# Kernel tuning notes

Measured on AMD Instinct MI355X. Metric: run time of the kernel, lower is better.

## Reference

```python
import jax, jax.numpy as jnp
import numpy as np
from itertools import permutations

NODE, BATCH, DIM, STEP = 32, 64, 32, 8
E = NODE * (NODE - 1)          # 992 directed edges (all ordered pairs)
K = 3                          # edge types
MSG_HID = 64; MSG_OUT = 64; N_HID = 64; PRED_LEN = 8


def setup_inputs() -> dict:
    key = jax.random.key(0)
    ks = jax.random.split(key, 12)
    es = jnp.asarray(np.array(list(permutations(range(NODE), 2))).T, dtype=jnp.int32)  # [2, E]
    x = jax.random.normal(ks[0], (BATCH, NODE, DIM, STEP), jnp.float32)
    z = jax.nn.softmax(jax.random.normal(ks[1], (BATCH, E, K), jnp.float32), axis=-1)
    p = lambda k, shape: jax.random.normal(k, shape, jnp.float32) * 0.1
    return dict(
        x=x, z=z, es=es,
        nodes_mask=jnp.zeros((NODE,), jnp.float32),
        edges_mask=jnp.zeros((E,), jnp.float32),
        mask=jnp.zeros((1,), jnp.float32),
        msg_W1=p(ks[2], (K, 2 * DIM, MSG_HID)), msg_b1=jnp.zeros((K, MSG_HID), jnp.float32),
        msg_W2=p(ks[3], (K, MSG_HID, MSG_OUT)), msg_b2=jnp.zeros((K, MSG_OUT), jnp.float32),
        out_W1=p(ks[4], (DIM + MSG_OUT, N_HID)), out_b1=jnp.zeros((N_HID,), jnp.float32),
        out_W2=p(ks[5], (N_HID, N_HID)), out_b2=jnp.zeros((N_HID,), jnp.float32),
        out_W3=p(ks[6], (N_HID, DIM)), out_b3=jnp.zeros((DIM,), jnp.float32),
        ge_Wi=p(ks[7], (3, N_HID, N_HID)), ge_bi=jnp.zeros((3, N_HID), jnp.float32),
        ge_Wh=p(ks[8], (3, N_HID, N_HID)), ge_bh=jnp.zeros((3, N_HID), jnp.float32),
        gn_Wi=p(ks[9], (3, N_HID + DIM, N_HID + DIM)), gn_bi=jnp.zeros((3, N_HID + DIM), jnp.float32),
        gn_Wh=p(ks[10], (3, N_HID + DIM, N_HID + DIM)), gn_bh=jnp.zeros((3, N_HID + DIM), jnp.float32),
    )


def _gru(inp, hid, Wi, bi, Wh, bh):
    # GRUX: state defaults to hidden
    r = jax.nn.sigmoid(inp @ Wi[0] + bi[0] + hid @ Wh[0] + bh[0])
    i = jax.nn.sigmoid(inp @ Wi[1] + bi[1] + hid @ Wh[1] + bh[1])
    n = jnp.tanh(inp @ Wi[2] + bi[2] + r * (hid @ Wh[2] + bh[2]))
    return (1.0 - i) * n + i * hid


def _run(x, z, es, msg_W1, msg_b1, msg_W2, msg_b2,
         out_W1, out_b1, out_W2, out_b2, out_W3, out_b3,
         ge_Wi, ge_bi, ge_Wh, ge_bh, gn_Wi, gn_bi, gn_Wh, gn_bh):
    xp = jnp.transpose(x, (1, 0, 3, 2))   # [node, batch, step, dim]
    zp = jnp.transpose(z, (1, 0, 2))      # [E, batch, K]
    col, row = es[0], es[1]               # 'o2i': col,row = es; aggregate at col
    counts = jnp.clip(jax.ops.segment_sum(jnp.ones((E,), x.dtype), col, num_segments=NODE), 1.0)
    h_node = h_edge = None
    x_m = None
    xs = []
    for t in range(STEP + PRED_LEN):
        x_in = xp[:, :, t, :] if t < STEP else x_m   # [node, batch, dim]
        # edge gather: msg = cat([x[row], x[col]])
        msg = jnp.concatenate([x_in[row], x_in[col]], axis=-1)  # [E, b, 2*dim]
        # per-edge-type 2-layer MLP mixture, weighted by z, normalized by K
        h1 = jax.nn.relu(jnp.einsum('ebi,kih->kebh', msg, msg_W1) + msg_b1[:, None, None, :])
        h2 = jax.nn.relu(jnp.einsum('kebh,kho->kebo', h1, msg_W2) + msg_b2[:, None, None, :])
        msgs = jnp.einsum('kebo,ebk->ebo', h2, zp) / K          # [E, b, msg_out]
        if h_edge is not None:
            msgs = _gru(msgs, h_edge, ge_Wi, ge_bi, ge_Wh, ge_bh)
        # scatter-mean to nodes
        agg = jax.ops.segment_sum(msgs, col, num_segments=NODE) / counts[:, None, None]
        cat = jnp.concatenate([x_in, agg], axis=-1)             # [node, b, dim+msg_out]
        if h_node is not None:
            cat = _gru(cat, h_node, gn_Wi, gn_bi, gn_Wh, gn_bh)
        h = jax.nn.relu(cat @ out_W1 + out_b1)
        h = jax.nn.relu(h @ out_W2 + out_b2)
        delta = h @ out_W3 + out_b3
        x_m = x_in + delta
        h_node, h_edge = cat, msgs
        xs.append(x_m)
    x_hat = jnp.transpose(jnp.stack(xs, axis=2), (1, 0, 3, 2))  # [batch, node, dim, T]
    return x_hat


def reference(x, z, es, nodes_mask, edges_mask, mask,
              msg_W1, msg_b1, msg_W2, msg_b2,
              out_W1, out_b1, out_W2, out_b2, out_W3, out_b3,
              ge_Wi, ge_bi, ge_Wh, ge_bh, gn_Wi, gn_bi, gn_Wh, gn_bh):
    x_hat = _run(x, z, es, msg_W1, msg_b1, msg_W2, msg_b2,
                 out_W1, out_b1, out_W2, out_b2, out_W3, out_b3,
                 ge_Wi, ge_bi, ge_Wh, ge_bh, gn_Wi, gn_bi, gn_Wh, gn_bh)
    return (x_hat[:, :, :, -PRED_LEN:], x_hat, x_hat)
```

## Files before the change

kernel.cpp:

```cpp
#include <hip/hip_runtime.h>
#include <hip/hip_bf16.h>

#define NNODE 32
#define NB    64
#define NDIM  32
#define NSTEP 8
#define NE    992
#define NTT   16

typedef __bf16 bf16;
typedef __attribute__((ext_vector_type(8))) __bf16 bf16x8;
typedef __attribute__((ext_vector_type(4))) __bf16 bf16x4;
typedef __attribute__((ext_vector_type(4))) float  f32x4;

__device__ __forceinline__ f32x4 mfma_bf16(bf16x8 a, bf16x8 b, f32x4 c) {
  return __builtin_amdgcn_mfma_f32_16x16x32_bf16(a, b, c, 0, 0, 0);
}
__device__ __forceinline__ float sigm(float x) { return 1.0f / (1.0f + __expf(-x)); }
__device__ __forceinline__ float tanh_f(float x) {
  x = fminf(fmaxf(x, -15.0f), 15.0f);
  float e = __expf(2.0f * x);
  return (e - 1.0f) / (e + 1.0f);
}

__global__ void prep_weights(
    const float* __restrict__ msgW1, const float* __restrict__ msgW2,
    const float* __restrict__ geWi,  const float* __restrict__ geWh,
    const float* __restrict__ gnWi,  const float* __restrict__ gnWh,
    const float* __restrict__ oW1,   const float* __restrict__ oW2,
    const float* __restrict__ oW3,
    bf16* __restrict__ B1, bf16* __restrict__ B2,
    bf16* __restrict__ GI, bf16* __restrict__ GH,
    bf16* __restrict__ GN,
    bf16* __restrict__ OW1s, bf16* __restrict__ OW2s, bf16* __restrict__ OW3s) {
  int u = blockIdx.x * 256 + threadIdx.x;
  if (u < 12288) {
    int k = u >> 12, i = (u >> 6) & 63, h = u & 63;
    int kf = i >> 5, quad = (i >> 3) & 3, j = i & 7;
    int nn = k * 64 + h, nt = nn >> 4, lane = quad * 16 + (nn & 15);
    int slot = ((nt * 2 + kf) * 64 + lane) * 8 + j;
    B1[slot] = (bf16)msgW1[u];
    GI[slot] = (bf16)geWi[u];
    GH[slot] = (bf16)geWh[u];
    int ntl = h >> 4, lane2 = quad * 16 + (h & 15);
    int slot2 = k * 4096 + ((ntl * 2 + kf) * 64 + lane2) * 8 + j;
    B2[slot2] = (bf16)msgW2[u];
  } else if (u < 39936) {
    int v = u - 12288;
    int kk = v / 9216, rem = v % 9216, i = rem / 96, h = rem % 96;
    int kf = i >> 5, loc = i & 31, quad = loc >> 3, j = loc & 7;
    int nn = kk * 96 + h, nt = nn >> 4, lane = quad * 16 + (nn & 15);
    int slot = ((nt * 3 + kf) * 64 + lane) * 8 + j;
    GN[slot]         = (bf16)gnWi[v];
    GN[27648 + slot] = (bf16)gnWh[v];
  } else if (u < 46080) {
    int v = u - 39936; int i = v >> 6, h = v & 63;
    int kf = i >> 5, loc = i & 31, quad = loc >> 3, j = loc & 7;
    int nt = h >> 4, lane = quad * 16 + (h & 15);
    OW1s[((nt * 3 + kf) * 64 + lane) * 8 + j] = (bf16)oW1[v];
  } else if (u < 50176) {
    int v = u - 46080; int i = v >> 6, h = v & 63;
    int kf = i >> 5, quad = (i >> 3) & 3, j = i & 7;
    int nt = h >> 4, lane = quad * 16 + (h & 15);
    OW2s[((nt * 2 + kf) * 64 + lane) * 8 + j] = (bf16)oW2[v];
  } else if (u < 52224) {
    int v = u - 50176; int i = v >> 5, h = v & 31;
    int kf = i >> 5, quad = (i >> 3) & 3, j = i & 7;
    int nt = h >> 4, lane = quad * 16 + (h & 15);
    OW3s[((nt * 2 + kf) * 64 + lane) * 8 + j] = (bf16)oW3[v];
  }
}

__global__ void copy_x(const float* __restrict__ x, float* __restrict__ xf,
                       bf16* __restrict__ xb) {
  int u = blockIdx.x * 256 + threadIdx.x;
  int n = u >> 11, b = (u >> 5) & 63, d = u & 31;
  float v = x[((b * 32 + n) * 32 + d) * 8 + 0];
  xf[u] = v;
  xb[u] = (bf16)v;
}

__global__ __launch_bounds__(512, 4) void edge_step(
    const bf16* __restrict__ xb, const int* __restrict__ es,
    const float* __restrict__ z,
    const bf16* __restrict__ B1, const bf16* __restrict__ B2,
    const float* __restrict__ mb1, const float* __restrict__ mb2,
    const bf16* __restrict__ GI, const bf16* __restrict__ GH,
    const float* __restrict__ gbi, const float* __restrict__ gbh,
    bf16* __restrict__ hed, int t) {
  __shared__ __align__(16) char scrbuf[51200];
  __shared__ float zL[2][64][3];
  __shared__ __align__(16) bf16 Hh[2][64][72];
  bf16 (*A)[64][72]   = (bf16(*)[64][72])scrbuf;
  bf16 (*A2)[64][200] = (bf16(*)[64][200])scrbuf;

  int e0 = blockIdx.x * 2, tid = threadIdx.x;
  int c0_ = es[e0],     r0 = es[NE + e0];
  int c1_ = es[e0 + 1], r1 = es[NE + e0 + 1];
  int wv = tid >> 6, ln = tid & 63, quad = ln >> 4, l16 = ln & 15;
  int rg = wv & 3, cg = wv >> 2;
  int m = rg * 16 + l16;

  for (int u = tid; u < 384; u += 512) {
    int pe = u / 192, rem = u % 192, b = rem / 3, k = rem % 3;
    zL[pe][b][k] = z[(b * NE + e0 + pe) * 3 + k];
  }
  if (t > 0) {
    for (int u = tid; u < 1024; u += 512) {
      int pe = u >> 9, c = u & 511;
      int b = c >> 3, j = c & 7;
      *(bf16x8*)&Hh[pe][b][j * 8] =
          *(const bf16x8*)(hed + (e0 + pe) * 4096 + b * 64 + j * 8);
    }
  }

  bf16x8 af[2][2];
  af[0][0] = *(const bf16x8*)(xb + r0 * 2048 + m * 32 + quad * 8);
  af[0][1] = *(const bf16x8*)(xb + c0_ * 2048 + m * 32 + quad * 8);
  af[1][0] = *(const bf16x8*)(xb + r1 * 2048 + m * 32 + quad * 8);
  af[1][1] = *(const bf16x8*)(xb + c1_ * 2048 + m * 32 + quad * 8);

  f32x4 acc1[2][6];
#pragma unroll
  for (int pe = 0; pe < 2; pe++)
#pragma unroll
    for (int q = 0; q < 6; q++) { f32x4 zz = {0.f,0.f,0.f,0.f}; acc1[pe][q] = zz; }
#pragma unroll
  for (int j = 0; j < 6; j++) {
    int nt = cg * 6 + j;
    bf16x8 w0 = *(const bf16x8*)&B1[(nt * 2 + 0) * 512 + ln * 8];
    bf16x8 w1 = *(const bf16x8*)&B1[(nt * 2 + 1) * 512 + ln * 8];
#pragma unroll
    for (int pe = 0; pe < 2; pe++) {
      acc1[pe][j] = mfma_bf16(af[pe][0], w0, acc1[pe][j]);
      acc1[pe][j] = mfma_bf16(af[pe][1], w1, acc1[pe][j]);
    }
  }
#pragma unroll
  for (int j = 0; j < 6; j++) {
    int nt = cg * 6 + j;
    int n = nt * 16 + l16;
    float bias = mb1[n];
#pragma unroll
    for (int pe = 0; pe < 2; pe++)
#pragma unroll
      for (int r = 0; r < 4; r++) {
        float v = acc1[pe][j][r] + bias;
        A2[pe][rg * 16 + quad * 4 + r][n] = (bf16)(v > 0.f ? v : 0.f);
      }
  }
  __syncthreads();
  f32x4 acc2[2][3][2];
#pragma unroll
  for (int pe = 0; pe < 2; pe++)
#pragma unroll
    for (int kt = 0; kt < 3; kt++)
#pragma unroll
      for (int oi = 0; oi < 2; oi++) { f32x4 zz = {0.f,0.f,0.f,0.f}; acc2[pe][kt][oi] = zz; }
#pragma unroll
  for (int kt = 0; kt < 3; kt++) {
    bf16x8 a2f[2][2];
#pragma unroll
    for (int pe = 0; pe < 2; pe++)
#pragma unroll
      for (int kf = 0; kf < 2; kf++)
        a2f[pe][kf] = *(const bf16x8*)&A2[pe][m][kt * 64 + kf * 32 + quad * 8];
#pragma unroll
    for (int oi = 0; oi < 2; oi++) {
      int ot = cg * 2 + oi;
      bf16x8 w0 = *(const bf16x8*)&B2[kt * 4096 + (ot * 2 + 0) * 512 + ln * 8];
      bf16x8 w1 = *(const bf16x8*)&B2[kt * 4096 + (ot * 2 + 1) * 512 + ln * 8];
#pragma unroll
      for (int pe = 0; pe < 2; pe++) {
        acc2[pe][kt][oi] = mfma_bf16(a2f[pe][0], w0, acc2[pe][kt][oi]);
        acc2[pe][kt][oi] = mfma_bf16(a2f[pe][1], w1, acc2[pe][kt][oi]);
      }
    }
  }
  __syncthreads();
  float mb2v[3][2];
#pragma unroll
  for (int kt = 0; kt < 3; kt++)
#pragma unroll
    for (int oi = 0; oi < 2; oi++)
      mb2v[kt][oi] = mb2[kt * 64 + (cg * 2 + oi) * 16 + l16];
#pragma unroll
  for (int pe = 0; pe < 2; pe++)
#pragma unroll
    for (int r = 0; r < 4; r++) {
      int b = rg * 16 + quad * 4 + r;
      float z0 = zL[pe][b][0], z1 = zL[pe][b][1], z2 = zL[pe][b][2];
#pragma unroll
      for (int oi = 0; oi < 2; oi++) {
        int o = (cg * 2 + oi) * 16 + l16;
        float h0 = acc2[pe][0][oi][r] + mb2v[0][oi]; h0 = h0 > 0.f ? h0 : 0.f;
        float h1 = acc2[pe][1][oi][r] + mb2v[1][oi]; h1 = h1 > 0.f ? h1 : 0.f;
        float h2 = acc2[pe][2][oi][r] + mb2v[2][oi]; h2 = h2 > 0.f ? h2 : 0.f;
        float val = (h0 * z0 + h1 * z1 + h2 * z2) * (1.0f / 3.0f);
        if (t == 0)
          hed[(e0 + pe) * 4096 + b * 64 + o] = (bf16)val;
        else
          A[pe][b][o] = (bf16)val;
      }
    }
  if (t > 0) {
    __syncthreads();
    bf16x8 ai[2][2], ah[2][2];
#pragma unroll
    for (int pe = 0; pe < 2; pe++)
#pragma unroll
      for (int kf = 0; kf < 2; kf++) {
        ai[pe][kf] = *(const bf16x8*)&A[pe][m][kf * 32 + quad * 8];
        ah[pe][kf] = *(const bf16x8*)&Hh[pe][m][kf * 32 + quad * 8];
      }
#pragma unroll
    for (int oi = 0; oi < 2; oi++) {
      int ot = cg * 2 + oi;
      f32x4 gr[2], gi2[2], gni2[2], gnh2[2];
#pragma unroll
      for (int pe = 0; pe < 2; pe++) {
        f32x4 zz = {0.f,0.f,0.f,0.f};
        gr[pe] = zz; gi2[pe] = zz; gni2[pe] = zz; gnh2[pe] = zz;
      }
#pragma unroll
      for (int g = 0; g < 2; g++) {
        int nt = g * 4 + ot;
        bf16x8 wi0 = *(const bf16x8*)&GI[(nt * 2 + 0) * 512 + ln * 8];
        bf16x8 wi1 = *(const bf16x8*)&GI[(nt * 2 + 1) * 512 + ln * 8];
        bf16x8 wh0 = *(const bf16x8*)&GH[(nt * 2 + 0) * 512 + ln * 8];
        bf16x8 wh1 = *(const bf16x8*)&GH[(nt * 2 + 1) * 512 + ln * 8];
#pragma unroll
        for (int pe = 0; pe < 2; pe++) {
          f32x4 a = g ? gi2[pe] : gr[pe];
          a = mfma_bf16(ai[pe][0], wi0, a);
          a = mfma_bf16(ai[pe][1], wi1, a);
          a = mfma_bf16(ah[pe][0], wh0, a);
          a = mfma_bf16(ah[pe][1], wh1, a);
          if (g) gi2[pe] = a; else gr[pe] = a;
        }
      }
      {
        int nt = 8 + ot;
        bf16x8 wi0 = *(const bf16x8*)&GI[(nt * 2 + 0) * 512 + ln * 8];
        bf16x8 wi1 = *(const bf16x8*)&GI[(nt * 2 + 1) * 512 + ln * 8];
        bf16x8 wh0 = *(const bf16x8*)&GH[(nt * 2 + 0) * 512 + ln * 8];
        bf16x8 wh1 = *(const bf16x8*)&GH[(nt * 2 + 1) * 512 + ln * 8];
#pragma unroll
        for (int pe = 0; pe < 2; pe++) {
          gni2[pe] = mfma_bf16(ai[pe][0], wi0, gni2[pe]);
          gni2[pe] = mfma_bf16(ai[pe][1], wi1, gni2[pe]);
          gnh2[pe] = mfma_bf16(ah[pe][0], wh0, gnh2[pe]);
          gnh2[pe] = mfma_bf16(ah[pe][1], wh1, gnh2[pe]);
        }
      }
      int o = ot * 16 + l16;
      float bir = gbi[o],       bhr = gbh[o];
      float bii = gbi[64 + o],  bhi = gbh[64 + o];
      float bin = gbi[128 + o], bhn = gbh[128 + o];
#pragma unroll
      for (int pe = 0; pe < 2; pe++)
#pragma unroll
        for (int r = 0; r < 4; r++) {
          int b = rg * 16 + quad * 4 + r;
          float xr = gr[pe][r]   + bir + bhr;
          float xi = gi2[pe][r]  + bii + bhi;
          float xn = gni2[pe][r] + bin;
          float hn = gnh2[pe][r] + bhn;
          float rgt = sigm(xr);
          float ig  = sigm(xi);
          float ng  = tanh_f(xn + rgt * hn);
          float hv  = (float)Hh[pe][b][o];
          hed[(e0 + pe) * 4096 + b * 64 + o] =
              (bf16)((1.0f - ig) * ng + ig * hv);
        }
    }
  }
}

__global__ __launch_bounds__(256) void node_kernel(
    const float* __restrict__ x, const bf16* __restrict__ hed,
    float* __restrict__ xf, bf16* __restrict__ xb, float* __restrict__ hnode,
    const bf16* __restrict__ GN,
    const float* __restrict__ gnbi, const float* __restrict__ gnbh,
    const bf16* __restrict__ OW1, const float* __restrict__ ob1,
    const bf16* __restrict__ OW2, const float* __restrict__ ob2,
    const bf16* __restrict__ OW3, const float* __restrict__ ob3,
    float* __restrict__ out, int t) {
  __shared__ float aggf[16][64];
  __shared__ float xinf[16][32];
  __shared__ float hvf[16][96];
  __shared__ __align__(16) bf16 c0b[16][112];
  __shared__ __align__(16) bf16 hvb[16][112];
  __shared__ float gsum[2][16][290];
  __shared__ __align__(16) bf16 cnb[16][112];
  __shared__ __align__(16) bf16 s1b[16][112];
  __shared__ __align__(16) bf16 s2b[16][112];
  int nq = blockIdx.x, n = nq >> 2, q = nq & 3;
  int tid = threadIdx.x;
  {
    int r = tid >> 4, o4 = tid & 15;
    const bf16x4* bp = (const bf16x4*)hed + (size_t)n * 31 * 1024 + (q * 16 + r) * 16 + o4;
    float sx = 0.f, sy = 0.f, sz = 0.f, sw = 0.f;
#pragma unroll
    for (int e2 = 0; e2 < 31; e2++) {
      bf16x4 v = bp[e2 * 1024];
      sx += (float)v[0]; sy += (float)v[1]; sz += (float)v[2]; sw += (float)v[3];
    }
    const float inv = 1.0f / 31.0f;
    sx *= inv; sy *= inv; sz *= inv; sw *= inv;
    int o = o4 * 4;
    aggf[r][o] = sx; aggf[r][o + 1] = sy; aggf[r][o + 2] = sz; aggf[r][o + 3] = sw;
    c0b[r][32 + o] = (bf16)sx; c0b[r][33 + o] = (bf16)sy;
    c0b[r][34 + o] = (bf16)sz; c0b[r][35 + o] = (bf16)sw;
  }
  if (tid < 128) {
    int r = tid >> 3, d0 = (tid & 7) * 4;
    int b = q * 16 + r;
#pragma unroll
    for (int k = 0; k < 4; k++) {
      float v = xf[n * 2048 + b * 32 + d0 + k];
      xinf[r][d0 + k] = v;
      c0b[r][d0 + k] = (bf16)v;
    }
  }
  if (t > 0) {
    int r = tid >> 4, cb = (tid & 15) * 6;
    int row = n * 64 + q * 16 + r;
#pragma unroll
    for (int k = 0; k < 6; k++) {
      float v = hnode[row * 96 + cb + k];
      hvf[r][cb + k] = v;
      hvb[r][cb + k] = (bf16)v;
    }
  }
  __syncthreads();
  int wv = tid >> 6, ln = tid & 63, quad = ln >> 4, l16 = ln & 15;
  if (t > 0) {
    int mat = wv >> 1, sel = wv & 1;
    const bf16(*Ab)[112] = mat ? hvb : c0b;
    bf16x8 af[3];
#pragma unroll
    for (int kf = 0; kf < 3; kf++)
      af[kf] = *(const bf16x8*)&Ab[l16][kf * 32 + quad * 8];
    const bf16* W = GN + mat * 27648;
    f32x4 accn[9];
#pragma unroll
    for (int q2 = 0; q2 < 9; q2++) { f32x4 zz = {0.f,0.f,0.f,0.f}; accn[q2] = zz; }
#pragma unroll
    for (int nt2 = 0; nt2 < 9; nt2++) {
      int nt = sel * 9 + nt2;
#pragma unroll
      for (int kf = 0; kf < 3; kf++) {
        bf16x8 bfrag = *(const bf16x8*)&W[((nt * 3 + kf) * 64 + ln) * 8];
        accn[nt2] = mfma_bf16(af[kf], bfrag, accn[nt2]);
      }
    }
#pragma unroll
    for (int nt2 = 0; nt2 < 9; nt2++) {
      int col = (sel * 9 + nt2) * 16 + l16;
#pragma unroll
      for (int rr = 0; rr < 4; rr++)
        gsum[mat][quad * 4 + rr][col] = accn[nt2][rr];
    }
  }
  __syncthreads();
  {
    int r = tid >> 4, cb = (tid & 15) * 6;
    int row = n * 64 + q * 16 + r;
#pragma unroll
    for (int k = 0; k < 6; k++) {
      int c = cb + k;
      float v;
      if (t > 0) {
        float xr = gsum[0][r][c] + gnbi[c] + gsum[1][r][c] + gnbh[c];
        float xi = gsum[0][r][96 + c] + gnbi[96 + c] + gsum[1][r][96 + c] + gnbh[96 + c];
        float xn = gsum[0][r][192 + c] + gnbi[192 + c];
        float hn = gsum[1][r][192 + c] + gnbh[192 + c];
        float rg = sigm(xr);
        float ig = sigm(xi);
        float ng = tanh_f(xn + rg * hn);
        v = (1.0f - ig) * ng + ig * hvf[r][c];
      } else {
        v = (c < 32) ? xinf[r][c] : aggf[r][c - 32];
      }
      cnb[r][c] = (bf16)v;
      hnode[row * 96 + c] = v;
    }
  }
  __syncthreads();
  {
    bf16x8 af3[3];
#pragma unroll
    for (int kf = 0; kf < 3; kf++)
      af3[kf] = *(const bf16x8*)&cnb[l16][kf * 32 + quad * 8];
    f32x4 accn = {0.f, 0.f, 0.f, 0.f};
#pragma unroll
    for (int kf = 0; kf < 3; kf++) {
      bf16x8 bfrag = *(const bf16x8*)&OW1[((wv * 3 + kf) * 64 + ln) * 8];
      accn = mfma_bf16(af3[kf], bfrag, accn);
    }
    int col = wv * 16 + l16;
    float bias = ob1[col];
#pragma unroll
    for (int rr = 0; rr < 4; rr++) {
      float vv = accn[rr] + bias;
      s1b[quad * 4 + rr][col] = (bf16)(vv > 0.f ? vv : 0.f);
    }
  }
  __syncthreads();
  {
    bf16x8 af2[2];
#pragma unroll
    for (int kf = 0; kf < 2; kf++)
      af2[kf] = *(const bf16x8*)&s1b[l16][kf * 32 + quad * 8];
    f32x4 accn = {0.f, 0.f, 0.f, 0.f};
#pragma unroll
    for (int kf = 0; kf < 2; kf++) {
      bf16x8 bfrag = *(const bf16x8*)&OW2[((wv * 2 + kf) * 64 + ln) * 8];
      accn = mfma_bf16(af2[kf], bfrag, accn);
    }
    int col = wv * 16 + l16;
    float bias = ob2[col];
#pragma unroll
    for (int rr = 0; rr < 4; rr++) {
      float vv = accn[rr] + bias;
      s2b[quad * 4 + rr][col] = (bf16)(vv > 0.f ? vv : 0.f);
    }
  }
  __syncthreads();
  if (wv < 2) {
    bf16x8 af2[2];
#pragma unroll
    for (int kf = 0; kf < 2; kf++)
      af2[kf] = *(const bf16x8*)&s2b[l16][kf * 32 + quad * 8];
    f32x4 accn = {0.f, 0.f, 0.f, 0.f};
#pragma unroll
    for (int kf = 0; kf < 2; kf++) {
      bf16x8 bfrag = *(const bf16x8*)&OW3[((wv * 2 + kf) * 64 + ln) * 8];
      accn = mfma_bf16(af2[kf], bfrag, accn);
    }
    int d = wv * 16 + l16;
    float bias = ob3[d];
#pragma unroll
    for (int rr = 0; rr < 4; rr++) {
      int r = quad * 4 + rr;
      int b = q * 16 + r;
      float xm = xinf[r][d] + accn[rr] + bias;
      int base = (b * 32 + n) * 32 + d;
      out[524288 + base * 16 + t] = xm;
      out[1572864 + base * 16 + t] = xm;
      if (t >= NSTEP) out[base * 8 + (t - NSTEP)] = xm;
      float vnext = (t + 1 < NSTEP) ? x[base * 8 + (t + 1)] : xm;
      xf[n * 2048 + b * 32 + d] = vnext;
      xb[n * 2048 + b * 32 + d] = (bf16)vnext;
    }
  }
}

extern "C" void kernel_launch(void* const* d_in, const int* in_sizes, int n_in,
                              void* d_out, int out_size, void* d_ws, size_t ws_size,
                              hipStream_t stream) {
  const float* x     = (const float*)d_in[0];
  const float* z     = (const float*)d_in[1];
  const int*   es    = (const int*)d_in[2];
  const float* msgW1 = (const float*)d_in[6];
  const float* msgb1 = (const float*)d_in[7];
  const float* msgW2 = (const float*)d_in[8];
  const float* msgb2 = (const float*)d_in[9];
  const float* oW1   = (const float*)d_in[10];
  const float* ob1   = (const float*)d_in[11];
  const float* oW2   = (const float*)d_in[12];
  const float* ob2   = (const float*)d_in[13];
  const float* oW3   = (const float*)d_in[14];
  const float* ob3   = (const float*)d_in[15];
  const float* geWi  = (const float*)d_in[16];
  const float* gebi  = (const float*)d_in[17];
  const float* geWh  = (const float*)d_in[18];
  const float* gebh  = (const float*)d_in[19];
  const float* gnWi  = (const float*)d_in[20];
  const float* gnbi  = (const float*)d_in[21];
  const float* gnWh  = (const float*)d_in[22];
  const float* gnbh  = (const float*)d_in[23];
  float* out = (float*)d_out;

  char* p = (char*)d_ws;
  bf16*  hed   = (bf16*)p;   p += (size_t)NE * 4096 * 2;
  float* xf    = (float*)p;  p += 65536 * 4;
  bf16*  xb    = (bf16*)p;   p += 65536 * 2;
  float* hnode = (float*)p;  p += 196608 * 4;
  bf16*  B1sw  = (bf16*)p;   p += 12288 * 2;
  bf16*  B2sw  = (bf16*)p;   p += 12288 * 2;
  bf16*  GIsw  = (bf16*)p;   p += 12288 * 2;
  bf16*  GHsw  = (bf16*)p;   p += 12288 * 2;
  bf16*  GNsw  = (bf16*)p;   p += 55296 * 2;
  bf16*  OW1s  = (bf16*)p;   p += 6144 * 2;
  bf16*  OW2s  = (bf16*)p;   p += 4096 * 2;
  bf16*  OW3s  = (bf16*)p;   p += 2048 * 2;

  prep_weights<<<204, 256, 0, stream>>>(msgW1, msgW2, geWi, geWh, gnWi, gnWh,
                                        oW1, oW2, oW3,
                                        B1sw, B2sw, GIsw, GHsw, GNsw,
                                        OW1s, OW2s, OW3s);
  copy_x<<<256, 256, 0, stream>>>(x, xf, xb);

  for (int t = 0; t < NTT; t++) {
    edge_step<<<NE / 2, 512, 0, stream>>>(xb, es, z, B1sw, B2sw, msgb1, msgb2,
                                          GIsw, GHsw, gebi, gebh, hed, t);
    node_kernel<<<128, 256, 0, stream>>>(x, hed, xf, xb, hnode, GNsw, gnbi, gnbh,
                                         OW1s, ob1, OW2s, ob2, OW3s, ob3,
                                         out, t);
  }
}
```

Baseline: 599.7 us.

## Fuse edge-to-node scatter-sum into edge kernel via float atomics

The edge kernel now atomically adds each bf16-rounded edge message into a float per-node aggregation buffer, indexed by the edge's target node. The node kernel then reads one float4 from that buffer, instead of summing 31 edge messages from the hed array, and zeroes it for the next step. The buffer is zeroed once in copy_x. This removes the 31-way strided gather from the node kernel. In exchange the edge kernel issues about 4M contended float atomics per step, and float atomic order makes the summation order nondeterministic.

```diff
diff --git a/kernel.cpp b/kernel.cpp
--- a/kernel.cpp
+++ b/kernel.cpp
@@ -72,8 +72,10 @@
 }
 
 __global__ void copy_x(const float* __restrict__ x, float* __restrict__ xf,
-                       bf16* __restrict__ xb) {
+                       bf16* __restrict__ xb, float* __restrict__ agg) {
   int u = blockIdx.x * 256 + threadIdx.x;
+  agg[u] = 0.f;
+  agg[u + 65536] = 0.f;
   int n = u >> 11, b = (u >> 5) & 63, d = u & 31;
   float v = x[((b * 32 + n) * 32 + d) * 8 + 0];
   xf[u] = v;
@@ -87,7 +89,7 @@
     const float* __restrict__ mb1, const float* __restrict__ mb2,
     const bf16* __restrict__ GI, const bf16* __restrict__ GH,
     const float* __restrict__ gbi, const float* __restrict__ gbh,
-    bf16* __restrict__ hed, int t) {
+    bf16* __restrict__ hed, float* __restrict__ agg, int t) {
   __shared__ __align__(16) char scrbuf[51200];
   __shared__ float zL[2][64][3];
   __shared__ __align__(16) bf16 Hh[2][64][72];
@@ -197,10 +199,13 @@
         float h1 = acc2[pe][1][oi][r] + mb2v[1][oi]; h1 = h1 > 0.f ? h1 : 0.f;
         float h2 = acc2[pe][2][oi][r] + mb2v[2][oi]; h2 = h2 > 0.f ? h2 : 0.f;
         float val = (h0 * z0 + h1 * z1 + h2 * z2) * (1.0f / 3.0f);
-        if (t == 0)
-          hed[(e0 + pe) * 4096 + b * 64 + o] = (bf16)val;
-        else
+        if (t == 0) {
+          bf16 bv = (bf16)val;
+          hed[(e0 + pe) * 4096 + b * 64 + o] = bv;
+          atomicAdd(&agg[((pe ? c1_ : c0_) * 64 + b) * 64 + o], (float)bv);
+        } else {
           A[pe][b][o] = (bf16)val;
+        }
       }
     }
   if (t > 0) {
@@ -270,15 +275,16 @@
           float ig  = sigm(xi);
           float ng  = tanh_f(xn + rgt * hn);
           float hv  = (float)Hh[pe][b][o];
-          hed[(e0 + pe) * 4096 + b * 64 + o] =
-              (bf16)((1.0f - ig) * ng + ig * hv);
+          bf16 bv = (bf16)((1.0f - ig) * ng + ig * hv);
+          hed[(e0 + pe) * 4096 + b * 64 + o] = bv;
+          atomicAdd(&agg[((pe ? c1_ : c0_) * 64 + b) * 64 + o], (float)bv);
         }
     }
   }
 }
 
 __global__ __launch_bounds__(256) void node_kernel(
-    const float* __restrict__ x, const bf16* __restrict__ hed,
+    const float* __restrict__ x, float* __restrict__ agg,
     float* __restrict__ xf, bf16* __restrict__ xb, float* __restrict__ hnode,
     const bf16* __restrict__ GN,
     const float* __restrict__ gnbi, const float* __restrict__ gnbh,
@@ -299,15 +305,12 @@
   int tid = threadIdx.x;
   {
     int r = tid >> 4, o4 = tid & 15;
-    const bf16x4* bp = (const bf16x4*)hed + (size_t)n * 31 * 1024 + (q * 16 + r) * 16 + o4;
-    float sx = 0.f, sy = 0.f, sz = 0.f, sw = 0.f;
-#pragma unroll
-    for (int e2 = 0; e2 < 31; e2++) {
-      bf16x4 v = bp[e2 * 1024];
-      sx += (float)v[0]; sy += (float)v[1]; sz += (float)v[2]; sw += (float)v[3];
-    }
+    float* ap = agg + ((size_t)(n * 64) + q * 16 + r) * 64 + o4 * 4;
+    f32x4 s = *(const f32x4*)ap;
+    f32x4 zz = {0.f, 0.f, 0.f, 0.f};
+    *(f32x4*)ap = zz;
     const float inv = 1.0f / 31.0f;
-    sx *= inv; sy *= inv; sz *= inv; sw *= inv;
+    float sx = s[0] * inv, sy = s[1] * inv, sz = s[2] * inv, sw = s[3] * inv;
     int o = o4 * 4;
     aggf[r][o] = sx; aggf[r][o + 1] = sy; aggf[r][o + 2] = sz; aggf[r][o + 3] = sw;
     c0b[r][32 + o] = (bf16)sx; c0b[r][33 + o] = (bf16)sy;
@@ -488,6 +491,7 @@
   float* xf    = (float*)p;  p += 65536 * 4;
   bf16*  xb    = (bf16*)p;   p += 65536 * 2;
   float* hnode = (float*)p;  p += 196608 * 4;
+  float* agg   = (float*)p;  p += 131072 * 4;
   bf16*  B1sw  = (bf16*)p;   p += 12288 * 2;
   bf16*  B2sw  = (bf16*)p;   p += 12288 * 2;
   bf16*  GIsw  = (bf16*)p;   p += 12288 * 2;
@@ -501,12 +505,12 @@
                                         oW1, oW2, oW3,
                                         B1sw, B2sw, GIsw, GHsw, GNsw,
                                         OW1s, OW2s, OW3s);
-  copy_x<<<256, 256, 0, stream>>>(x, xf, xb);
+  copy_x<<<256, 256, 0, stream>>>(x, xf, xb, agg);
 
   for (int t = 0; t < NTT; t++) {
     edge_step<<<NE / 2, 512, 0, stream>>>(xb, es, z, B1sw, B2sw, msgb1, msgb2,
-                                          GIsw, GHsw, gebi, gebh, hed, t);
-    node_kernel<<<128, 256, 0, stream>>>(x, hed, xf, xb, hnode, GNsw, gnbi, gnbh,
+                                          GIsw, GHsw, gebi, gebh, hed, agg, t);
+    node_kernel<<<128, 256, 0, stream>>>(x, agg, xf, xb, hnode, GNsw, gnbi, gnbh,
                                          OW1s, ob1, OW2s, ob2, OW3s, ob3,
                                          out, t);
   }
```

Result: slower. 618.8 us (+3.2%).

## Fuse node step t-1 with edge step t during teacher-forced phase

Applied to the files above, without the earlier changes.

Because teacher-forced edge inputs come directly from x, the edge step for t no longer depends on the node step for t-1. The change double-buffers the edge hidden state, precomputes bf16 x for all input steps, and launches one fused kernel whose first blocks run node work while the rest run edge work. This aims to remove a launch and serialization gap per teacher-forced step and overlap the small node grid with edge work. It enlarges the static shared memory of edge blocks, which may lower occupancy, and adds a second hidden-state buffer.

```diff
diff --git a/kernel.cpp b/kernel.cpp
--- a/kernel.cpp
+++ b/kernel.cpp
@@ -72,29 +72,31 @@
 }
 
 __global__ void copy_x(const float* __restrict__ x, float* __restrict__ xf,
-                       bf16* __restrict__ xb) {
+                       bf16* __restrict__ xball) {
   int u = blockIdx.x * 256 + threadIdx.x;
   int n = u >> 11, b = (u >> 5) & 63, d = u & 31;
-  float v = x[((b * 32 + n) * 32 + d) * 8 + 0];
-  xf[u] = v;
-  xb[u] = (bf16)v;
-}
-
-__global__ __launch_bounds__(512, 4) void edge_step(
-    const bf16* __restrict__ xb, const int* __restrict__ es,
+  int base = ((b * 32 + n) * 32 + d) * 8;
+  xf[u] = x[base];
+#pragma unroll
+  for (int t = 0; t < 8; t++)
+    xball[t * 65536 + u] = (bf16)x[base + t];
+}
+
+__device__ __forceinline__ void edge_body(
+    char* smem, int e0, int tid,
+    const bf16* __restrict__ xsrc, const int* __restrict__ es,
     const float* __restrict__ z,
     const bf16* __restrict__ B1, const bf16* __restrict__ B2,
     const float* __restrict__ mb1, const float* __restrict__ mb2,
     const bf16* __restrict__ GI, const bf16* __restrict__ GH,
     const float* __restrict__ gbi, const float* __restrict__ gbh,
-    bf16* __restrict__ hed, int t) {
-  __shared__ __align__(16) char scrbuf[51200];
-  __shared__ float zL[2][64][3];
-  __shared__ __align__(16) bf16 Hh[2][64][72];
+    const bf16* __restrict__ hedR, bf16* __restrict__ hedW, int t) {
+  char* scrbuf = smem;
+  float (*zL)[64][3] = (float(*)[64][3])(smem + 51200);
+  bf16 (*Hh)[64][72] = (bf16(*)[64][72])(smem + 52736);
   bf16 (*A)[64][72]   = (bf16(*)[64][72])scrbuf;
   bf16 (*A2)[64][200] = (bf16(*)[64][200])scrbuf;
 
-  int e0 = blockIdx.x * 2, tid = threadIdx.x;
   int c0_ = es[e0],     r0 = es[NE + e0];
   int c1_ = es[e0 + 1], r1 = es[NE + e0 + 1];
   int wv = tid >> 6, ln = tid & 63, quad = ln >> 4, l16 = ln & 15;
@@ -110,15 +112,15 @@
       int pe = u >> 9, c = u & 511;
       int b = c >> 3, j = c & 7;
       *(bf16x8*)&Hh[pe][b][j * 8] =
-          *(const bf16x8*)(hed + (e0 + pe) * 4096 + b * 64 + j * 8);
+          *(const bf16x8*)(hedR + (e0 + pe) * 4096 + b * 64 + j * 8);
     }
   }
 
   bf16x8 af[2][2];
-  af[0][0] = *(const bf16x8*)(xb + r0 * 2048 + m * 32 + quad * 8);
-  af[0][1] = *(const bf16x8*)(xb + c0_ * 2048 + m * 32 + quad * 8);
-  af[1][0] = *(const bf16x8*)(xb + r1 * 2048 + m * 32 + quad * 8);
-  af[1][1] = *(const bf16x8*)(xb + c1_ * 2048 + m * 32 + quad * 8);
+  af[0][0] = *(const bf16x8*)(xsrc + r0 * 2048 + m * 32 + quad * 8);
+  af[0][1] = *(const bf16x8*)(xsrc + c0_ * 2048 + m * 32 + quad * 8);
+  af[1][0] = *(const bf16x8*)(xsrc + r1 * 2048 + m * 32 + quad * 8);
+  af[1][1] = *(const bf16x8*)(xsrc + c1_ * 2048 + m * 32 + quad * 8);
 
   f32x4 acc1[2][6];
 #pragma unroll
@@ -198,7 +200,7 @@
         float h2 = acc2[pe][2][oi][r] + mb2v[2][oi]; h2 = h2 > 0.f ? h2 : 0.f;
         float val = (h0 * z0 + h1 * z1 + h2 * z2) * (1.0f / 3.0f);
         if (t == 0)
-          hed[(e0 + pe) * 4096 + b * 64 + o] = (bf16)val;
+          hedW[(e0 + pe) * 4096 + b * 64 + o] = (bf16)val;
         else
           A[pe][b][o] = (bf16)val;
       }
@@ -270,14 +272,15 @@
           float ig  = sigm(xi);
           float ng  = tanh_f(xn + rgt * hn);
           float hv  = (float)Hh[pe][b][o];
-          hed[(e0 + pe) * 4096 + b * 64 + o] =
+          hedW[(e0 + pe) * 4096 + b * 64 + o] =
               (bf16)((1.0f - ig) * ng + ig * hv);
         }
     }
   }
 }
 
-__global__ __launch_bounds__(256) void node_kernel(
+__device__ __forceinline__ void node_body(
+    char* smem, int nq, int tid,
     const float* __restrict__ x, const bf16* __restrict__ hed,
     float* __restrict__ xf, bf16* __restrict__ xb, float* __restrict__ hnode,
     const bf16* __restrict__ GN,
@@ -286,18 +289,18 @@
     const bf16* __restrict__ OW2, const float* __restrict__ ob2,
     const bf16* __restrict__ OW3, const float* __restrict__ ob3,
     float* __restrict__ out, int t) {
-  __shared__ float aggf[16][64];
-  __shared__ float xinf[16][32];
-  __shared__ float hvf[16][96];
-  __shared__ __align__(16) bf16 c0b[16][112];
-  __shared__ __align__(16) bf16 hvb[16][112];
-  __shared__ float gsum[2][16][290];
-  __shared__ __align__(16) bf16 cnb[16][112];
-  __shared__ __align__(16) bf16 s1b[16][112];
-  __shared__ __align__(16) bf16 s2b[16][112];
-  int nq = blockIdx.x, n = nq >> 2, q = nq & 3;
-  int tid = threadIdx.x;
-  {
+  float (*aggf)[64]      = (float(*)[64])(smem);
+  float (*xinf)[32]      = (float(*)[32])(smem + 4096);
+  float (*hvf)[96]       = (float(*)[96])(smem + 6144);
+  bf16  (*c0b)[112]      = (bf16(*)[112])(smem + 12288);
+  bf16  (*hvb)[112]      = (bf16(*)[112])(smem + 15872);
+  float (*gsum)[16][290] = (float(*)[16][290])(smem + 19456);
+  bf16  (*cnb)[112]      = (bf16(*)[112])(smem + 56576);
+  bf16  (*s1b)[112]      = (bf16(*)[112])(smem + 60160);
+  bf16  (*s2b)[112]      = (bf16(*)[112])(smem + 63744);
+  int n = nq >> 2, q = nq & 3;
+  int wv = tid >> 6, ln = tid & 63, quad = ln >> 4, l16 = ln & 15;
+  if (tid < 256) {
     int r = tid >> 4, o4 = tid & 15;
     const bf16x4* bp = (const bf16x4*)hed + (size_t)n * 31 * 1024 + (q * 16 + r) * 16 + o4;
     float sx = 0.f, sy = 0.f, sz = 0.f, sw = 0.f;
@@ -323,7 +326,7 @@
       c0b[r][d0 + k] = (bf16)v;
     }
   }
-  if (t > 0) {
+  if (t > 0 && tid < 256) {
     int r = tid >> 4, cb = (tid & 15) * 6;
     int row = n * 64 + q * 16 + r;
 #pragma unroll
@@ -334,8 +337,7 @@
     }
   }
   __syncthreads();
-  int wv = tid >> 6, ln = tid & 63, quad = ln >> 4, l16 = ln & 15;
-  if (t > 0) {
+  if (t > 0 && wv < 4) {
     int mat = wv >> 1, sel = wv & 1;
     const bf16(*Ab)[112] = mat ? hvb : c0b;
     bf16x8 af[3];
@@ -364,7 +366,7 @@
     }
   }
   __syncthreads();
-  {
+  if (tid < 256) {
     int r = tid >> 4, cb = (tid & 15) * 6;
     int row = n * 64 + q * 16 + r;
 #pragma unroll
@@ -388,7 +390,7 @@
     }
   }
   __syncthreads();
-  {
+  if (wv < 4) {
     bf16x8 af3[3];
 #pragma unroll
     for (int kf = 0; kf < 3; kf++)
@@ -408,7 +410,7 @@
     }
   }
   __syncthreads();
-  {
+  if (wv < 4) {
     bf16x8 af2[2];
 #pragma unroll
     for (int kf = 0; kf < 2; kf++)
@@ -454,6 +456,59 @@
       xf[n * 2048 + b * 32 + d] = vnext;
       xb[n * 2048 + b * 32 + d] = (bf16)vnext;
     }
+  }
+}
+
+__global__ __launch_bounds__(512, 4) void edge_step(
+    const bf16* __restrict__ xsrc, const int* __restrict__ es,
+    const float* __restrict__ z,
+    const bf16* __restrict__ B1, const bf16* __restrict__ B2,
+    const float* __restrict__ mb1, const float* __restrict__ mb2,
+    const bf16* __restrict__ GI, const bf16* __restrict__ GH,
+    const float* __restrict__ gbi, const float* __restrict__ gbh,
+    const bf16* __restrict__ hedR, bf16* __restrict__ hedW, int t) {
+  __shared__ __align__(16) char smem[71168];
+  edge_body(smem, blockIdx.x * 2, threadIdx.x, xsrc, es, z, B1, B2, mb1, mb2,
+            GI, GH, gbi, gbh, hedR, hedW, t);
+}
+
+__global__ __launch_bounds__(256) void node_kernel(
+    const float* __restrict__ x, const bf16* __restrict__ hed,
+    float* __restrict__ xf, bf16* __restrict__ xb, float* __restrict__ hnode,
+    const bf16* __restrict__ GN,
+    const float* __restrict__ gnbi, const float* __restrict__ gnbh,
+    const bf16* __restrict__ OW1, const float* __restrict__ ob1,
+    const bf16* __restrict__ OW2, const float* __restrict__ ob2,
+    const bf16* __restrict__ OW3, const float* __restrict__ ob3,
+    float* __restrict__ out, int t) {
+  __shared__ __align__(16) char smem[67328];
+  node_body(smem, blockIdx.x, threadIdx.x, x, hed, xf, xb, hnode, GN,
+            gnbi, gnbh, OW1, ob1, OW2, ob2, OW3, ob3, out, t);
+}
+
+__global__ __launch_bounds__(512, 4) void fused_ne(
+    const float* __restrict__ x,
+    const bf16* __restrict__ xsrc, const int* __restrict__ es,
+    const float* __restrict__ z,
+    const bf16* __restrict__ B1, const bf16* __restrict__ B2,
+    const float* __restrict__ mb1, const float* __restrict__ mb2,
+    const bf16* __restrict__ GI, const bf16* __restrict__ GH,
+    const float* __restrict__ gbi, const float* __restrict__ gbh,
+    const bf16* __restrict__ hedR, bf16* __restrict__ hedW,
+    float* __restrict__ xf, bf16* __restrict__ xb, float* __restrict__ hnode,
+    const bf16* __restrict__ GN,
+    const float* __restrict__ gnbi, const float* __restrict__ gnbh,
+    const bf16* __restrict__ OW1, const float* __restrict__ ob1,
+    const bf16* __restrict__ OW2, const float* __restrict__ ob2,
+    const bf16* __restrict__ OW3, const float* __restrict__ ob3,
+    float* __restrict__ out, int te) {
+  __shared__ __align__(16) char smem[71168];
+  if (blockIdx.x < 128) {
+    node_body(smem, blockIdx.x, threadIdx.x, x, hedR, xf, xb, hnode, GN,
+              gnbi, gnbh, OW1, ob1, OW2, ob2, OW3, ob3, out, te - 1);
+  } else {
+    edge_body(smem, (blockIdx.x - 128) * 2, threadIdx.x, xsrc, es, z, B1, B2,
+              mb1, mb2, GI, GH, gbi, gbh, hedR, hedW, te);
   }
 }
 
@@ -484,7 +539,9 @@
   float* out = (float*)d_out;
 
   char* p = (char*)d_ws;
-  bf16*  hed   = (bf16*)p;   p += (size_t)NE * 4096 * 2;
+  bf16*  hedA  = (bf16*)p;   p += (size_t)NE * 4096 * 2;
+  bf16*  hedB  = (bf16*)p;   p += (size_t)NE * 4096 * 2;
+  bf16*  xball = (bf16*)p;   p += (size_t)8 * 65536 * 2;
   float* xf    = (float*)p;  p += 65536 * 4;
   bf16*  xb    = (bf16*)p;   p += 65536 * 2;
   float* hnode = (float*)p;  p += 196608 * 4;
@@ -497,17 +554,34 @@
   bf16*  OW2s  = (bf16*)p;   p += 4096 * 2;
   bf16*  OW3s  = (bf16*)p;   p += 2048 * 2;
 
+  bf16* hbuf[2] = {hedA, hedB};
+
   prep_weights<<<204, 256, 0, stream>>>(msgW1, msgW2, geWi, geWh, gnWi, gnWh,
                                         oW1, oW2, oW3,
                                         B1sw, B2sw, GIsw, GHsw, GNsw,
                                         OW1s, OW2s, OW3s);
-  copy_x<<<256, 256, 0, stream>>>(x, xf, xb);
-
-  for (int t = 0; t < NTT; t++) {
+  copy_x<<<256, 256, 0, stream>>>(x, xf, xball);
+
+  edge_step<<<NE / 2, 512, 0, stream>>>(xball, es, z, B1sw, B2sw, msgb1, msgb2,
+                                        GIsw, GHsw, gebi, gebh,
+                                        hbuf[1], hbuf[0], 0);
+  for (int t = 1; t < NSTEP; t++) {
+    fused_ne<<<128 + NE / 2, 512, 0, stream>>>(
+        x, xball + (size_t)t * 65536, es, z, B1sw, B2sw, msgb1, msgb2,
+        GIsw, GHsw, gebi, gebh,
+        hbuf[(t - 1) & 1], hbuf[t & 1],
+        xf, xb, hnode, GNsw, gnbi, gnbh,
+        OW1s, ob1, OW2s, ob2, OW3s, ob3, out, t);
+  }
+  node_kernel<<<128, 256, 0, stream>>>(x, hbuf[(NSTEP - 1) & 1], xf, xb, hnode,
+                                       GNsw, gnbi, gnbh, OW1s, ob1, OW2s, ob2,
+                                       OW3s, ob3, out, NSTEP - 1);
+  for (int t = NSTEP; t < NTT; t++) {
     edge_step<<<NE / 2, 512, 0, stream>>>(xb, es, z, B1sw, B2sw, msgb1, msgb2,
-                                          GIsw, GHsw, gebi, gebh, hed, t);
-    node_kernel<<<128, 256, 0, stream>>>(x, hed, xf, xb, hnode, GNsw, gnbi, gnbh,
-                                         OW1s, ob1, OW2s, ob2, OW3s, ob3,
-                                         out, t);
-  }
-}
+                                          GIsw, GHsw, gebi, gebh,
+                                          hbuf[(t - 1) & 1], hbuf[t & 1], t);
+    node_kernel<<<128, 256, 0, stream>>>(x, hbuf[t & 1], xf, xb, hnode,
+                                         GNsw, gnbi, gnbh, OW1s, ob1, OW2s, ob2,
+                                         OW3s, ob3, out, t);
+  }
+}
```

After: 553.5 us (median of 2 runs). 1.08x faster.
